# Performance work log

Measured on AMD Instinct MI355X. Metric: run time of the kernel, lower is better.

The kernel has to match this reference:

```python
import jax, jax.numpy as jnp
import numpy as np

N_NODES = 32768


def setup_inputs() -> dict:
    key = jax.random.key(0)
    ks = jax.random.split(key, 6)
    x = jax.random.normal(ks[0], (N_NODES, 128), dtype=jnp.float32)
    edge_index = jax.random.randint(ks[1], (2, 262144), 0, N_NODES, dtype=jnp.int64)
    weights = jax.random.normal(ks[2], (64, 128, 128), dtype=jnp.float32) * (1.0 / np.sqrt(128.0))
    biases = jax.random.normal(ks[3], (64, 128), dtype=jnp.float32) * 0.02
    cls_w = jax.random.normal(ks[4], (128, 4), dtype=jnp.float32) * (1.0 / np.sqrt(128.0))
    cls_b = jax.random.normal(ks[5], (4,), dtype=jnp.float32) * 0.02
    return {"x": x, "edge_index": edge_index, "weights": weights,
            "biases": biases, "cls_w": cls_w, "cls_b": cls_b}


def reference(x, edge_index, weights, biases, cls_w, cls_b):
    n = x.shape[0]
    # GCN normalization with self-loops (PyG GCNConv default):
    # A_hat = D^-1/2 (A + I) D^-1/2, deg counted on target nodes.
    loop = jnp.arange(n, dtype=edge_index.dtype)
    src = jnp.concatenate([edge_index[0], loop])  # [E+N]
    dst = jnp.concatenate([edge_index[1], loop])  # [E+N]
    deg = jax.ops.segment_sum(jnp.ones_like(dst, dtype=x.dtype), dst, num_segments=n)
    dinv = jnp.where(deg > 0, jax.lax.rsqrt(deg), 0.0)
    norm = dinv[src] * dinv[dst]  # [E+N]

    def gcn_layer(h, wb):
        W, b = wb
        hw = h @ W                                   # [N, H] dense transform
        msg = hw[src] * norm[:, None]                # gather + edge scaling
        agg = jax.ops.segment_sum(msg, dst, num_segments=n)  # scatter-add
        return jax.nn.relu(agg + b), None            # dropout is identity (eval)

    h, _ = jax.lax.scan(gcn_layer, x, (weights, biases))
    out = (h + x) @ cls_w + cls_b  # residual + linear classifier
    return out
```

## Files before the change

### kernel.cpp

```cpp
#include <hip/hip_runtime.h>
#include <hip/hip_bf16.h>

#define NN 32768
#define EE 262144
#define FD 128
#define NL 64
#define MROW 16
#define SROW 132

typedef short v8s __attribute__((ext_vector_type(8)));
typedef float v4f __attribute__((ext_vector_type(4)));

__device__ __forceinline__ unsigned short f2bf(float x) {
    unsigned u = __builtin_bit_cast(unsigned, x);
    u += 0x7fffu + ((u >> 16) & 1u);
    return (unsigned short)(u >> 16);
}
__device__ __forceinline__ float bf2f(unsigned short h) {
    unsigned u = ((unsigned)h) << 16;
    return __builtin_bit_cast(float, u);
}
__device__ __forceinline__ void acc8_bf16(float* acc, v8s r) {
    const int* d = (const int*)&r;
#pragma unroll
    for (int k = 0; k < 4; k++) {
        unsigned u = (unsigned)d[k];
        acc[2 * k]     += __builtin_bit_cast(float, u << 16);
        acc[2 * k + 1] += __builtin_bit_cast(float, u & 0xffff0000u);
    }
}

__global__ __launch_bounds__(256) void k_deg(const int* __restrict__ dst,
                                             int* __restrict__ cnt) {
    int e = blockIdx.x * 256 + threadIdx.x;
    if (e < EE) atomicAdd(&cnt[dst[e]], 1);
}

__global__ __launch_bounds__(256) void k_dinv(const int* __restrict__ cnt,
                                              float* __restrict__ dinv) {
    int i = blockIdx.x * 256 + threadIdx.x;
    if (i < NN) dinv[i] = rsqrtf((float)cnt[i] + 1.0f);
}

__global__ __launch_bounds__(256) void k_scanA(const int* __restrict__ cnt,
                                               int* __restrict__ bsum) {
    __shared__ int ws[4];
    int tid = threadIdx.x;
    int v = cnt[blockIdx.x * 256 + tid];
    int x = v;
#pragma unroll
    for (int off = 1; off < 64; off <<= 1) x += __shfl_xor(x, off);
    if ((tid & 63) == 0) ws[tid >> 6] = x;
    __syncthreads();
    if (tid == 0) bsum[blockIdx.x] = ws[0] + ws[1] + ws[2] + ws[3];
}
__global__ __launch_bounds__(128) void k_scanB(const int* __restrict__ bsum,
                                               int* __restrict__ boff,
                                               int* __restrict__ offs) {
    __shared__ int s0;
    int tid = threadIdx.x;
    int v = bsum[tid];
    int lane = tid & 63, w = tid >> 6;
    int x = v;
#pragma unroll
    for (int off = 1; off < 64; off <<= 1) {
        int y = __shfl_up(x, off);
        if (lane >= off) x += y;
    }
    if (tid == 63) s0 = x;
    __syncthreads();
    int excl = x - v + (w ? s0 : 0);
    boff[tid] = excl;
    if (tid == 127) offs[NN] = excl + v;
}
__global__ __launch_bounds__(256) void k_scanC(const int* __restrict__ cnt,
                                               const int* __restrict__ boff,
                                               int* __restrict__ offs) {
    __shared__ int ws[4];
    int tid = threadIdx.x;
    int i = blockIdx.x * 256 + tid;
    int v = cnt[i];
    int lane = tid & 63, w = tid >> 6;
    int x = v;
#pragma unroll
    for (int off = 1; off < 64; off <<= 1) {
        int y = __shfl_up(x, off);
        if (lane >= off) x += y;
    }
    if (lane == 63) ws[w] = x;
    __syncthreads();
    int wexcl = 0;
#pragma unroll
    for (int k = 0; k < 4; k++) if (k < w) wexcl += ws[k];
    offs[i] = boff[blockIdx.x] + wexcl + x - v;
}

__global__ __launch_bounds__(256) void k_fill(const int* __restrict__ src,
                                              const int* __restrict__ dst,
                                              const int* __restrict__ offs,
                                              int* __restrict__ cursor,
                                              int* __restrict__ col) {
    int e = blockIdx.x * 256 + threadIdx.x;
    if (e >= EE) return;
    int s = src[e], d = dst[e];
    int slot = atomicAdd(&cursor[d], 1);
    col[offs[d] + slot] = s;
}

__global__ __launch_bounds__(256) void k_xcast(const float* __restrict__ x,
                                               const float* __restrict__ dinv,
                                               unsigned short* __restrict__ g) {
    int i = blockIdx.x * 256 + threadIdx.x;
    float di = dinv[(i * 8) >> 7];
    float4 a = *(const float4*)(x + (size_t)i * 8);
    float4 b = *(const float4*)(x + (size_t)i * 8 + 4);
    v8s o;
    o[0] = (short)f2bf(di * a.x); o[1] = (short)f2bf(di * a.y);
    o[2] = (short)f2bf(di * a.z); o[3] = (short)f2bf(di * a.w);
    o[4] = (short)f2bf(di * b.x); o[5] = (short)f2bf(di * b.y);
    o[6] = (short)f2bf(di * b.z); o[7] = (short)f2bf(di * b.w);
    *(v8s*)(g + (size_t)i * 8) = o;
}

__global__ __launch_bounds__(256) void k_wcast(const float* __restrict__ W,
                                               unsigned short* __restrict__ Whi) {
    int t = blockIdx.x * 256 + threadIdx.x;
    int l = t >> 11;
    int rem = t & 2047;
    int ks = rem >> 9;
    int rem2 = rem & 511;
    int nt = rem2 >> 6;
    int L = rem2 & 63;
    const float* Wl = W + (size_t)l * FD * FD;
    int kbase = ks * 32 + ((L >> 4) << 3);
    int n = nt * 16 + (L & 15);
    v8s hv;
#pragma unroll
    for (int j = 0; j < 8; j++)
        hv[j] = (short)f2bf(Wl[(size_t)(kbase + j) * FD + n]);
    *(v8s*)(Whi + (size_t)t * 8) = hv;
}

__global__ __launch_bounds__(256, 8) void k_layer(
        const unsigned short* __restrict__ g,
        const int* __restrict__ offs,
        const int* __restrict__ col,
        const unsigned short* __restrict__ Whi,
        const float* __restrict__ dinv,
        const float* __restrict__ bias,
        unsigned short* __restrict__ gout,
        int last) {
    __shared__ unsigned short sA[MROW * SROW];
    __shared__ float sDinv[MROW];
    int tid = threadIdx.x;
    int lane = tid & 63;
    int w = tid >> 6;
    int row0 = blockIdx.x * MROW;
    int fg = lane >> 4;
    int fl = lane & 15;
    const unsigned short* gf = g + fl * 8;

    if (tid < MROW) sDinv[tid] = dinv[row0 + tid];

    int nbase = row0 + w * 4;
    int4 ov = *(const int4*)(offs + nbase);
    int o4 = offs[nbase + 4];
    int B0 = ov.x;
    int Etot = o4 - B0;

    if (Etot <= 64) {
        int c = (lane < Etot) ? col[B0 + lane] : 0;
        int node = nbase + fg;
        int sg = ((fg == 0) ? ov.x : (fg == 1) ? ov.y : (fg == 2) ? ov.z : ov.w) - B0;
        int eg = ((fg == 0) ? ov.y : (fg == 1) ? ov.z : (fg == 2) ? ov.w : o4) - B0;
        int len = eg - sg;
        int m = max(len, __shfl_xor(len, 16));
        m = max(m, __shfl_xor(m, 32));
        float acc[8];
#pragma unroll
        for (int k = 0; k < 8; k++) acc[k] = 0.f;
        for (int j = 0; j < m; j += 6) {
            int i0 = sg + j,     i1 = sg + j + 1, i2 = sg + j + 2;
            int i3 = sg + j + 3, i4 = sg + j + 4, i5 = sg + j + 5;
            bool p0 = i0 < eg, p1 = i1 < eg, p2 = i2 < eg;
            bool p3 = i3 < eg, p4 = i4 < eg, p5 = i5 < eg;
            int s0 = __shfl(c, i0 & 63);
            int s1 = __shfl(c, i1 & 63);
            int s2 = __shfl(c, i2 & 63);
            int s3 = __shfl(c, i3 & 63);
            int s4 = __shfl(c, i4 & 63);
            int s5 = __shfl(c, i5 & 63);
            v8s r0, r1, r2, r3, r4, r5;
            if (p0) r0 = *(const v8s*)(gf + (size_t)s0 * FD);
            if (p1) r1 = *(const v8s*)(gf + (size_t)s1 * FD);
            if (p2) r2 = *(const v8s*)(gf + (size_t)s2 * FD);
            if (p3) r3 = *(const v8s*)(gf + (size_t)s3 * FD);
            if (p4) r4 = *(const v8s*)(gf + (size_t)s4 * FD);
            if (p5) r5 = *(const v8s*)(gf + (size_t)s5 * FD);
            if (p0) acc8_bf16(acc, r0);
            if (p1) acc8_bf16(acc, r1);
            if (p2) acc8_bf16(acc, r2);
            if (p3) acc8_bf16(acc, r3);
            if (p4) acc8_bf16(acc, r4);
            if (p5) acc8_bf16(acc, r5);
        }
        v8s selfv = *(const v8s*)(gf + (size_t)node * FD);
        acc8_bf16(acc, selfv);
        float di = dinv[node];
        unsigned pk[4];
#pragma unroll
        for (int k = 0; k < 4; k++) {
            pk[k] = (unsigned)f2bf(di * acc[2 * k]) |
                    ((unsigned)f2bf(di * acc[2 * k + 1]) << 16);
        }
        *(v8s*)&sA[(w * 4 + fg) * SROW + fl * 8] = *(v8s*)pk;
    } else {
        for (int r = 0; r < 4; r++) {
            int nloc = w * 4 + r;
            int node = row0 + nloc;
            float acc[8];
#pragma unroll
            for (int k = 0; k < 8; k++) acc[k] = 0.f;
            int b = offs[node], e = offs[node + 1];
            int deg = e - b;
            for (int base = 0; base < deg; base += 64) {
                int n = min(deg - base, 64);
                int c = (lane < n) ? col[b + base + lane] : 0;
                for (int j = 0; j < n; j += 8) {
                    int e0 = j + fg, e1 = j + 4 + fg;
                    int s0 = __shfl(c, e0 & 63);
                    int s1 = __shfl(c, e1 & 63);
                    bool p0 = e0 < n, p1 = e1 < n;
                    v8s r0, r1;
                    if (p0) r0 = *(const v8s*)(gf + (size_t)s0 * FD);
                    if (p1) r1 = *(const v8s*)(gf + (size_t)s1 * FD);
                    if (p0) acc8_bf16(acc, r0);
                    if (p1) acc8_bf16(acc, r1);
                }
            }
#pragma unroll
            for (int k = 0; k < 8; k++) {
                acc[k] += __shfl_xor(acc[k], 16);
                acc[k] += __shfl_xor(acc[k], 32);
            }
            v8s sv = *(const v8s*)(gf + (size_t)node * FD);
            acc8_bf16(acc, sv);
            if (fg == 0) {
                float di = dinv[node];
                unsigned pk[4];
#pragma unroll
                for (int k = 0; k < 4; k++) {
                    pk[k] = (unsigned)f2bf(di * acc[2 * k]) |
                            ((unsigned)f2bf(di * acc[2 * k + 1]) << 16);
                }
                *(v8s*)&sA[nloc * SROW + fl * 8] = *(v8s*)pk;
            }
        }
    }
    __syncthreads();

    v4f a0 = (v4f){0.f, 0.f, 0.f, 0.f};
    v4f a1 = (v4f){0.f, 0.f, 0.f, 0.f};
#pragma unroll
    for (int ks = 0; ks < 4; ks++) {
        v8s ah = *(const v8s*)&sA[(lane & 15) * SROW + ks * 32 + ((lane >> 4) << 3)];
        size_t bo0 = ((size_t)(ks * 8 + w * 2) * 64 + lane) * 8;
        size_t bo1 = ((size_t)(ks * 8 + w * 2 + 1) * 64 + lane) * 8;
        v8s bh0 = *(const v8s*)(Whi + bo0);
        v8s bh1 = *(const v8s*)(Whi + bo1);
        a0 = __builtin_amdgcn_mfma_f32_16x16x32_bf16(ah, bh0, a0, 0, 0, 0);
        a1 = __builtin_amdgcn_mfma_f32_16x16x32_bf16(ah, bh1, a1, 0, 0, 0);
    }
    __syncthreads();

    float bb0 = bias[w * 32 + (lane & 15)];
    float bb1 = bias[w * 32 + 16 + (lane & 15)];
#pragma unroll
    for (int nt = 0; nt < 2; nt++) {
        int col_l = w * 32 + nt * 16 + (lane & 15);
        float bb = nt ? bb1 : bb0;
        v4f a = nt ? a1 : a0;
#pragma unroll
        for (int rg = 0; rg < 4; rg++) {
            int row_l = ((lane >> 4) << 2) + rg;
            float v = fmaxf(a[rg] + bb, 0.f);
            if (!last) v *= sDinv[row_l];
            sA[row_l * SROW + col_l] = f2bf(v);
        }
    }
    __syncthreads();
    int orow = tid >> 4;
    int ocol = (tid & 15) * 8;
    *(v8s*)(gout + (size_t)(row0 + orow) * FD + ocol) =
        *(const v8s*)&sA[orow * SROW + ocol];
}

__global__ __launch_bounds__(256) void k_cls(const unsigned short* __restrict__ h,
                                             const float* __restrict__ x,
                                             const float* __restrict__ cw,
                                             const float* __restrict__ cb,
                                             float* __restrict__ out) {
    int gw = (blockIdx.x * 256 + threadIdx.x) >> 6;
    int lane = threadIdx.x & 63;
    size_t o = (size_t)gw * FD + lane * 2;
    ushort2 hh = *(const ushort2*)(h + o);
    float2 xv = *(const float2*)(x + o);
    float sx = bf2f(hh.x) + xv.x;
    float sy = bf2f(hh.y) + xv.y;
    float4 w0 = *(const float4*)(cw + (lane * 2) * 4);
    float4 w1 = *(const float4*)(cw + (lane * 2 + 1) * 4);
    float p0 = sx * w0.x + sy * w1.x;
    float p1 = sx * w0.y + sy * w1.y;
    float p2 = sx * w0.z + sy * w1.z;
    float p3 = sx * w0.w + sy * w1.w;
#pragma unroll
    for (int off = 32; off > 0; off >>= 1) {
        p0 += __shfl_down(p0, off);
        p1 += __shfl_down(p1, off);
        p2 += __shfl_down(p2, off);
        p3 += __shfl_down(p3, off);
    }
    if (lane == 0) {
        float4 r2 = make_float4(p0 + cb[0], p1 + cb[1], p2 + cb[2], p3 + cb[3]);
        *(float4*)(out + (size_t)gw * 4) = r2;
    }
}

extern "C" void kernel_launch(void* const* d_in, const int* in_sizes, int n_in,
                              void* d_out, int out_size, void* d_ws, size_t ws_size,
                              hipStream_t stream) {
    const float* x       = (const float*)d_in[0];
    const int* ei        = (const int*)d_in[1];
    const float* weights = (const float*)d_in[2];
    const float* biases  = (const float*)d_in[3];
    const float* cls_w   = (const float*)d_in[4];
    const float* cls_b   = (const float*)d_in[5];
    float* out = (float*)d_out;

    char* ws = (char*)d_ws;
    size_t off = 0;
    auto alloc = [&](size_t bytes) -> void* {
        off = (off + 255) & ~(size_t)255;
        void* p = ws + off;
        off += bytes;
        return p;
    };
    int*   cnt    = (int*)alloc((size_t)NN * 4);
    int*   cursor = (int*)alloc((size_t)NN * 4);
    float* dinv   = (float*)alloc((size_t)NN * 4);
    int*   offs   = (int*)alloc((size_t)(NN + 1) * 4);
    int*   bsum   = (int*)alloc((size_t)128 * 4);
    int*   boff   = (int*)alloc((size_t)128 * 4);
    int*   col    = (int*)alloc((size_t)EE * 4);
    unsigned short* Whi = (unsigned short*)alloc((size_t)NL * FD * FD * 2);
    unsigned short* h0  = (unsigned short*)alloc((size_t)NN * FD * 2);
    unsigned short* h1  = (unsigned short*)alloc((size_t)NN * FD * 2);

    const int* srcv = ei;
    const int* dstv = ei + EE;

    hipMemsetAsync(cnt, 0, (size_t)NN * 4, stream);
    hipMemsetAsync(cursor, 0, (size_t)NN * 4, stream);
    k_deg<<<EE / 256, 256, 0, stream>>>(dstv, cnt);
    k_dinv<<<NN / 256, 256, 0, stream>>>(cnt, dinv);
    k_scanA<<<128, 256, 0, stream>>>(cnt, bsum);
    k_scanB<<<1, 128, 0, stream>>>(bsum, boff, offs);
    k_scanC<<<128, 256, 0, stream>>>(cnt, boff, offs);
    k_fill<<<EE / 256, 256, 0, stream>>>(srcv, dstv, offs, cursor, col);
    k_wcast<<<NL * 2048 / 256, 256, 0, stream>>>(weights, Whi);
    k_xcast<<<NN * FD / 2048, 256, 0, stream>>>(x, dinv, h1);

    const unsigned short* gin = h1;
    for (int l = 0; l < NL; l++) {
        unsigned short* gout = (l & 1) ? h1 : h0;
        k_layer<<<NN / MROW, 256, 0, stream>>>(gin, offs, col,
                                               Whi + (size_t)l * FD * FD,
                                               dinv, biases + (size_t)l * FD,
                                               gout, l == NL - 1);
        gin = gout;
    }
    k_cls<<<NN * 64 / 256, 256, 0, stream>>>(gin, x, cls_w, cls_b, out);
}
```

Baseline: 1.008 ms.

## Double layer tile rows, fuse classifier into last layer, merge setup kernels

```diff
diff --git a/kernel.cpp b/kernel.cpp
--- a/kernel.cpp
+++ b/kernel.cpp
@@ -5,8 +5,9 @@
 #define EE 262144
 #define FD 128
 #define NL 64
-#define MROW 16
+#define MROW 32
 #define SROW 132
+#define NBLKL (NN / MROW)
 
 typedef short v8s __attribute__((ext_vector_type(8)));
 typedef float v4f __attribute__((ext_vector_type(4)));
@@ -34,12 +35,6 @@
                                              int* __restrict__ cnt) {
     int e = blockIdx.x * 256 + threadIdx.x;
     if (e < EE) atomicAdd(&cnt[dst[e]], 1);
-}
-
-__global__ __launch_bounds__(256) void k_dinv(const int* __restrict__ cnt,
-                                              float* __restrict__ dinv) {
-    int i = blockIdx.x * 256 + threadIdx.x;
-    if (i < NN) dinv[i] = rsqrtf((float)cnt[i] + 1.0f);
 }
 
 __global__ __launch_bounds__(256) void k_scanA(const int* __restrict__ cnt,
@@ -75,7 +70,8 @@
 }
 __global__ __launch_bounds__(256) void k_scanC(const int* __restrict__ cnt,
                                                const int* __restrict__ boff,
-                                               int* __restrict__ offs) {
+                                               int* __restrict__ offs,
+                                               float* __restrict__ dinv) {
     __shared__ int ws[4];
     int tid = threadIdx.x;
     int i = blockIdx.x * 256 + tid;
@@ -93,6 +89,7 @@
 #pragma unroll
     for (int k = 0; k < 4; k++) if (k < w) wexcl += ws[k];
     offs[i] = boff[blockIdx.x] + wexcl + x - v;
+    dinv[i] = rsqrtf((float)v + 1.0f);
 }
 
 __global__ __launch_bounds__(256) void k_fill(const int* __restrict__ src,
@@ -107,41 +104,43 @@
     col[offs[d] + slot] = s;
 }
 
-__global__ __launch_bounds__(256) void k_xcast(const float* __restrict__ x,
-                                               const float* __restrict__ dinv,
-                                               unsigned short* __restrict__ g) {
-    int i = blockIdx.x * 256 + threadIdx.x;
-    float di = dinv[(i * 8) >> 7];
-    float4 a = *(const float4*)(x + (size_t)i * 8);
-    float4 b = *(const float4*)(x + (size_t)i * 8 + 4);
-    v8s o;
-    o[0] = (short)f2bf(di * a.x); o[1] = (short)f2bf(di * a.y);
-    o[2] = (short)f2bf(di * a.z); o[3] = (short)f2bf(di * a.w);
-    o[4] = (short)f2bf(di * b.x); o[5] = (short)f2bf(di * b.y);
-    o[6] = (short)f2bf(di * b.z); o[7] = (short)f2bf(di * b.w);
-    *(v8s*)(g + (size_t)i * 8) = o;
-}
-
-__global__ __launch_bounds__(256) void k_wcast(const float* __restrict__ W,
-                                               unsigned short* __restrict__ Whi) {
-    int t = blockIdx.x * 256 + threadIdx.x;
-    int l = t >> 11;
-    int rem = t & 2047;
-    int ks = rem >> 9;
-    int rem2 = rem & 511;
-    int nt = rem2 >> 6;
-    int L = rem2 & 63;
-    const float* Wl = W + (size_t)l * FD * FD;
-    int kbase = ks * 32 + ((L >> 4) << 3);
-    int n = nt * 16 + (L & 15);
-    v8s hv;
-#pragma unroll
-    for (int j = 0; j < 8; j++)
-        hv[j] = (short)f2bf(Wl[(size_t)(kbase + j) * FD + n]);
-    *(v8s*)(Whi + (size_t)t * 8) = hv;
-}
-
-__global__ __launch_bounds__(256, 8) void k_layer(
+__global__ __launch_bounds__(256) void k_wxcast(const float* __restrict__ W,
+                                                unsigned short* __restrict__ Whi,
+                                                const float* __restrict__ x,
+                                                const float* __restrict__ dinv,
+                                                unsigned short* __restrict__ g) {
+    int b = blockIdx.x;
+    if (b < NL * 2048 / 256) {
+        int t = b * 256 + threadIdx.x;
+        int l = t >> 11;
+        int rem = t & 2047;
+        int ks = rem >> 9;
+        int rem2 = rem & 511;
+        int nt = rem2 >> 6;
+        int L = rem2 & 63;
+        const float* Wl = W + (size_t)l * FD * FD;
+        int kbase = ks * 32 + ((L >> 4) << 3);
+        int n = nt * 16 + (L & 15);
+        v8s hv;
+#pragma unroll
+        for (int j = 0; j < 8; j++)
+            hv[j] = (short)f2bf(Wl[(size_t)(kbase + j) * FD + n]);
+        *(v8s*)(Whi + (size_t)t * 8) = hv;
+    } else {
+        int i = (b - NL * 2048 / 256) * 256 + threadIdx.x;
+        float di = dinv[(i * 8) >> 7];
+        float4 a = *(const float4*)(x + (size_t)i * 8);
+        float4 c = *(const float4*)(x + (size_t)i * 8 + 4);
+        v8s o;
+        o[0] = (short)f2bf(di * a.x); o[1] = (short)f2bf(di * a.y);
+        o[2] = (short)f2bf(di * a.z); o[3] = (short)f2bf(di * a.w);
+        o[4] = (short)f2bf(di * c.x); o[5] = (short)f2bf(di * c.y);
+        o[6] = (short)f2bf(di * c.z); o[7] = (short)f2bf(di * c.w);
+        *(v8s*)(g + (size_t)i * 8) = o;
+    }
+}
+
+__global__ __launch_bounds__(512, 8) void k_layer(
         const unsigned short* __restrict__ g,
         const int* __restrict__ offs,
         const int* __restrict__ col,
@@ -149,6 +148,10 @@
         const float* __restrict__ dinv,
         const float* __restrict__ bias,
         unsigned short* __restrict__ gout,
+        const float* __restrict__ x,
+        const float* __restrict__ cw,
+        const float* __restrict__ cb,
+        float* __restrict__ out,
         int last) {
     __shared__ unsigned short sA[MROW * SROW];
     __shared__ float sDinv[MROW];
@@ -259,13 +262,15 @@
     }
     __syncthreads();
 
+    int rt = w >> 2;
+    int wc = w & 3;
     v4f a0 = (v4f){0.f, 0.f, 0.f, 0.f};
     v4f a1 = (v4f){0.f, 0.f, 0.f, 0.f};
 #pragma unroll
     for (int ks = 0; ks < 4; ks++) {
-        v8s ah = *(const v8s*)&sA[(lane & 15) * SROW + ks * 32 + ((lane >> 4) << 3)];
-        size_t bo0 = ((size_t)(ks * 8 + w * 2) * 64 + lane) * 8;
-        size_t bo1 = ((size_t)(ks * 8 + w * 2 + 1) * 64 + lane) * 8;
+        v8s ah = *(const v8s*)&sA[(rt * 16 + (lane & 15)) * SROW + ks * 32 + ((lane >> 4) << 3)];
+        size_t bo0 = ((size_t)(ks * 8 + wc * 2) * 64 + lane) * 8;
+        size_t bo1 = ((size_t)(ks * 8 + wc * 2 + 1) * 64 + lane) * 8;
         v8s bh0 = *(const v8s*)(Whi + bo0);
         v8s bh1 = *(const v8s*)(Whi + bo1);
         a0 = __builtin_amdgcn_mfma_f32_16x16x32_bf16(ah, bh0, a0, 0, 0, 0);
@@ -273,56 +278,55 @@
     }
     __syncthreads();
 
-    float bb0 = bias[w * 32 + (lane & 15)];
-    float bb1 = bias[w * 32 + 16 + (lane & 15)];
+    float bb0 = bias[wc * 32 + (lane & 15)];
+    float bb1 = bias[wc * 32 + 16 + (lane & 15)];
 #pragma unroll
     for (int nt = 0; nt < 2; nt++) {
-        int col_l = w * 32 + nt * 16 + (lane & 15);
+        int col_l = wc * 32 + nt * 16 + (lane & 15);
         float bb = nt ? bb1 : bb0;
         v4f a = nt ? a1 : a0;
 #pragma unroll
         for (int rg = 0; rg < 4; rg++) {
-            int row_l = ((lane >> 4) << 2) + rg;
+            int row_l = rt * 16 + ((lane >> 4) << 2) + rg;
             float v = fmaxf(a[rg] + bb, 0.f);
             if (!last) v *= sDinv[row_l];
             sA[row_l * SROW + col_l] = f2bf(v);
         }
     }
     __syncthreads();
-    int orow = tid >> 4;
-    int ocol = (tid & 15) * 8;
-    *(v8s*)(gout + (size_t)(row0 + orow) * FD + ocol) =
-        *(const v8s*)&sA[orow * SROW + ocol];
-}
-
-__global__ __launch_bounds__(256) void k_cls(const unsigned short* __restrict__ h,
-                                             const float* __restrict__ x,
-                                             const float* __restrict__ cw,
-                                             const float* __restrict__ cb,
-                                             float* __restrict__ out) {
-    int gw = (blockIdx.x * 256 + threadIdx.x) >> 6;
-    int lane = threadIdx.x & 63;
-    size_t o = (size_t)gw * FD + lane * 2;
-    ushort2 hh = *(const ushort2*)(h + o);
-    float2 xv = *(const float2*)(x + o);
-    float sx = bf2f(hh.x) + xv.x;
-    float sy = bf2f(hh.y) + xv.y;
-    float4 w0 = *(const float4*)(cw + (lane * 2) * 4);
-    float4 w1 = *(const float4*)(cw + (lane * 2 + 1) * 4);
-    float p0 = sx * w0.x + sy * w1.x;
-    float p1 = sx * w0.y + sy * w1.y;
-    float p2 = sx * w0.z + sy * w1.z;
-    float p3 = sx * w0.w + sy * w1.w;
-#pragma unroll
-    for (int off = 32; off > 0; off >>= 1) {
-        p0 += __shfl_down(p0, off);
-        p1 += __shfl_down(p1, off);
-        p2 += __shfl_down(p2, off);
-        p3 += __shfl_down(p3, off);
-    }
-    if (lane == 0) {
-        float4 r2 = make_float4(p0 + cb[0], p1 + cb[1], p2 + cb[2], p3 + cb[3]);
-        *(float4*)(out + (size_t)gw * 4) = r2;
+
+    if (!last) {
+        int orow = tid >> 4;
+        int ocol = (tid & 15) * 8;
+        *(v8s*)(gout + (size_t)(row0 + orow) * FD + ocol) =
+            *(const v8s*)&sA[orow * SROW + ocol];
+    } else {
+        int row = tid >> 4;
+        int t = tid & 15;
+        int nd = row0 + row;
+        const unsigned short* hr = &sA[row * SROW + t * 8];
+        const float* xr = x + (size_t)nd * FD + t * 8;
+        float xv[8];
+        *(float4*)&xv[0] = *(const float4*)xr;
+        *(float4*)&xv[4] = *(const float4*)(xr + 4);
+        float p0 = 0.f, p1 = 0.f, p2 = 0.f, p3 = 0.f;
+#pragma unroll
+        for (int j = 0; j < 8; j++) {
+            float s = bf2f(hr[j]) + xv[j];
+            float4 wv = *(const float4*)(cw + (size_t)(t * 8 + j) * 4);
+            p0 += s * wv.x; p1 += s * wv.y; p2 += s * wv.z; p3 += s * wv.w;
+        }
+#pragma unroll
+        for (int off = 1; off < 16; off <<= 1) {
+            p0 += __shfl_xor(p0, off);
+            p1 += __shfl_xor(p1, off);
+            p2 += __shfl_xor(p2, off);
+            p3 += __shfl_xor(p3, off);
+        }
+        if (t == 0) {
+            float4 r = make_float4(p0 + cb[0], p1 + cb[1], p2 + cb[2], p3 + cb[3]);
+            *(float4*)(out + (size_t)nd * 4) = r;
+        }
     }
 }
 
@@ -362,22 +366,21 @@
     hipMemsetAsync(cnt, 0, (size_t)NN * 4, stream);
     hipMemsetAsync(cursor, 0, (size_t)NN * 4, stream);
     k_deg<<<EE / 256, 256, 0, stream>>>(dstv, cnt);
-    k_dinv<<<NN / 256, 256, 0, stream>>>(cnt, dinv);
     k_scanA<<<128, 256, 0, stream>>>(cnt, bsum);
     k_scanB<<<1, 128, 0, stream>>>(bsum, boff, offs);
-    k_scanC<<<128, 256, 0, stream>>>(cnt, boff, offs);
+    k_scanC<<<128, 256, 0, stream>>>(cnt, boff, offs, dinv);
     k_fill<<<EE / 256, 256, 0, stream>>>(srcv, dstv, offs, cursor, col);
-    k_wcast<<<NL * 2048 / 256, 256, 0, stream>>>(weights, Whi);
-    k_xcast<<<NN * FD / 2048, 256, 0, stream>>>(x, dinv, h1);
+    k_wxcast<<<NL * 2048 / 256 + NN * FD / 2048, 256, 0, stream>>>(
+        weights, Whi, x, dinv, h1);
 
     const unsigned short* gin = h1;
     for (int l = 0; l < NL; l++) {
         unsigned short* gout = (l & 1) ? h1 : h0;
-        k_layer<<<NN / MROW, 256, 0, stream>>>(gin, offs, col,
-                                               Whi + (size_t)l * FD * FD,
-                                               dinv, biases + (size_t)l * FD,
-                                               gout, l == NL - 1);
+        k_layer<<<NBLKL, 512, 0, stream>>>(gin, offs, col,
+                                           Whi + (size_t)l * FD * FD,
+                                           dinv, biases + (size_t)l * FD,
+                                           gout, x, cls_w, cls_b, out,
+                                           l == NL - 1);
         gin = gout;
     }
-    k_cls<<<NN * 64 / 256, 256, 0, stream>>>(gin, x, cls_w, cls_b, out);
-}
+}
```

After: 1.029 ms. +2.0%, slower.
